# Optimization experiments

Hardware: AMD Instinct MI355X
Metric: run time of the kernel (lower is better)

The kernel has to match this reference:

```python
import jax, jax.numpy as jnp
import numpy as np

B, S, D = 4, 2048, 1024

def setup_inputs() -> dict:
    key = jax.random.key(0)
    ks = jax.random.split(key, 7)
    sc = 1.0 / np.sqrt(D)
    return {
        "x": jax.random.normal(ks[0], (B, S, D), dtype=jnp.float32),
        "Wq": jax.random.normal(ks[1], (D, D), dtype=jnp.float32) * sc,
        "bq": jax.random.normal(ks[2], (D,), dtype=jnp.float32) * 0.01,
        "Wk": jax.random.normal(ks[3], (D, D), dtype=jnp.float32) * sc,
        "bk": jax.random.normal(ks[4], (D,), dtype=jnp.float32) * 0.01,
        "Wv": jax.random.normal(ks[5], (D, D), dtype=jnp.float32) * sc,
        "bv": jax.random.normal(ks[6], (D,), dtype=jnp.float32) * 0.01,
    }

def reference(x, Wq, bq, Wk, bk, Wv, bv):
    # q, k, v: [B, S, D] projections (torch Linear: x @ W^T + b; here W stored as [in, out])
    q = jnp.einsum("bsd,df->bsf", x, Wq) + bq
    k = jnp.einsum("bsd,df->bsf", x, Wk) + bk
    v = jnp.einsum("bsd,df->bsf", x, Wv) + bv
    dim = x.shape[-1]
    # scores: [B, S, S], scaled by sqrt(full d_model) as in the source
    scores = jnp.einsum("bqd,bkd->bqk", q, k) / jnp.sqrt(jnp.float32(dim)).astype(x.dtype)
    attn = jax.nn.softmax(scores, axis=-1)
    return jnp.einsum("bqk,bkd->bqd", attn, v)
```

## Files before the change

kernel.cpp:

```cpp
#include <hip/hip_runtime.h>
#include <hip/hip_bf16.h>

typedef __attribute__((ext_vector_type(8))) short bf16x8;
typedef __attribute__((ext_vector_type(4))) float f32x4;
typedef unsigned short u16;

__device__ __forceinline__ u16 f2bf(float f) {
  unsigned int u = __builtin_bit_cast(unsigned int, f);
  u += 0x7fffu + ((u >> 16) & 1u);
  return (u16)(u >> 16);
}
__device__ __forceinline__ float bf2f(unsigned int h) {
  unsigned int u = h << 16;
  return __builtin_bit_cast(float, u);
}

__device__ __forceinline__ void gload_lds16(const void* g, void* l) {
  __builtin_amdgcn_global_load_lds(
      (const __attribute__((address_space(1))) void*)g,
      (__attribute__((address_space(3))) void*)l, 16, 0, 0);
}

#define BAR() __builtin_amdgcn_s_barrier()
#define VMC(N) asm volatile("s_waitcnt vmcnt(%0)" ::"n"(N) : "memory")

template <int EPI>
__global__ __launch_bounds__(512, 2) void gemm2t(
    const u16* __restrict__ Abase, const u16* __restrict__ Btbase,
    const float* __restrict__ p0, float* __restrict__ p1,
    const float* __restrict__ p2, void* __restrict__ out0,
    void* __restrict__ out1, int Kd, int ldc, long long sAz, long long sBz,
    long long sCz) {
  constexpr int ASZ = 16384;
  constexpr int BSZ = 32768;
  constexpr int BBASE = 2 * ASZ;
  __shared__ char lds[2 * ASZ + 3 * BSZ];

  const int gx = gridDim.x, gy = gridDim.y;
  const int nwg = gx * gy * gridDim.z;
  const int orig = blockIdx.x + gx * (blockIdx.y + gy * blockIdx.z);
  const int q = nwg >> 3, r = nwg & 7;
  const int xcd = orig & 7, loc = orig >> 3;
  const int wgid =
      (xcd < r ? xcd * (q + 1) : r * (q + 1) + (xcd - r) * q) + loc;
  const int bxi = wgid % gx;
  const int byi = (wgid / gx) % gy;
  const int z = wgid / (gx * gy);

  const int tid = threadIdx.x;
  const int w = tid >> 6, l = tid & 63;
  const int wr = w >> 2, wc = w & 3;
  const int lq = l >> 4, lr = l & 15;
  const int bm = byi * 128, bn = bxi * 256;
  const u16* A = Abase + (size_t)z * sAz;
  const u16* Bt = Btbase + (size_t)z * sBz;
  const int NT = Kd >> 6;

  const int kbp = ((tid & 7) ^ ((tid >> 3) & 7)) * 8;
  const int drow = tid >> 3;
  const u16* gA[2];
  const u16* gB[4];
#pragma unroll
  for (int u = 0; u < 2; ++u)
    gA[u] = A + (size_t)(bm + u * 64 + drow) * Kd + kbp;
#pragma unroll
  for (int u = 0; u < 4; ++u)
    gB[u] = Bt + (size_t)(bn + u * 64 + drow) * Kd + kbp;

  auto stageA = [&](int kt) {
    char* d = lds + (kt & 1) * ASZ + tid * 16;
#pragma unroll
    for (int u = 0; u < 2; ++u) gload_lds16(gA[u] + kt * 64, d + u * 8192);
  };
  auto stageB = [&](int kt) {
    char* d = lds + BBASE + (kt % 3) * BSZ + tid * 16;
#pragma unroll
    for (int u = 0; u < 4; ++u) gload_lds16(gB[u] + kt * 64, d + u * 8192);
  };

  const int rA = wr * 64 + lr;
  const int rB0 = wc * 64 + lr;
  int aoff[2];
#pragma unroll
  for (int kh = 0; kh < 2; ++kh)
    aoff[kh] = rA * 128 + (((kh * 4 + lq) ^ (rA & 7)) << 4);

  f32x4 acc[4][2][2] = {};
  bf16x8 a[2][4];
  bf16x8 bb[2][2][2];

  auto rdA = [&](int kt) {
    const char* p = lds + (kt & 1) * ASZ;
#pragma unroll
    for (int kh = 0; kh < 2; ++kh)
#pragma unroll
      for (int mf = 0; mf < 4; ++mf)
        a[kh][mf] = *(const bf16x8*)(p + aoff[kh] + mf * 2048);
  };
  auto rdB = [&](int kt) {
    const char* p = lds + BBASE + (kt % 3) * BSZ;
#pragma unroll
    for (int nh = 0; nh < 2; ++nh) {
      const int rB = rB0 + nh * 32;
#pragma unroll
      for (int kh = 0; kh < 2; ++kh) {
        const int o = rB * 128 + (((kh * 4 + lq) ^ (rB & 7)) << 4);
#pragma unroll
        for (int nf = 0; nf < 2; ++nf)
          bb[nh][kh][nf] = *(const bf16x8*)(p + o + nf * 2048);
      }
    }
  };
  auto mma = [&](int kh) {
    __builtin_amdgcn_s_setprio(1);
#pragma unroll
    for (int nh = 0; nh < 2; ++nh)
#pragma unroll
      for (int mf = 0; mf < 4; ++mf)
#pragma unroll
        for (int nf = 0; nf < 2; ++nf)
          acc[mf][nh][nf] = __builtin_amdgcn_mfma_f32_16x16x32_bf16(
              a[kh][mf], bb[nh][kh][nf], acc[mf][nh][nf], 0, 0, 0);
    __builtin_amdgcn_s_setprio(0);
  };

  stageB(0);
  stageA(0);
  stageB(1);
  stageA(1);
  VMC(6);
  BAR();

  for (int t = 0; t < NT; ++t) {
    rdA(t);
    rdB(t);
    if (t + 2 < NT) stageB(t + 2);
    BAR();
    mma(0);
    if (t + 2 < NT) VMC(4); else VMC(0);
    BAR();
    if (t + 2 < NT) stageA(t + 2);
    mma(1);
  }

  if constexpr (EPI == 4) {
    constexpr float K2 = 0.045084834f;
    u16* C = (u16*)out0 + (size_t)z * sCz;
    const float* cc = p0 + z * 2048;
    float* rs = p1 + z * 2048;
    float psum[4][4] = {};
#pragma unroll
    for (int nh = 0; nh < 2; ++nh)
#pragma unroll
      for (int nf = 0; nf < 2; ++nf) {
        const int col = bn + wc * 64 + nh * 32 + nf * 16 + lr;
        const float cj2 = cc[col];
#pragma unroll
        for (int mf = 0; mf < 4; ++mf) {
          const int row = bm + wr * 64 + mf * 16 + lq * 4;
#pragma unroll
          for (int e = 0; e < 4; ++e) {
            const float pv = exp2f(fmaf(acc[mf][nh][nf][e], K2, cj2));
            C[(size_t)(row + e) * ldc + col] = f2bf(pv);
            psum[mf][e] += pv;
          }
        }
      }
#pragma unroll
    for (int off = 1; off <= 8; off <<= 1)
#pragma unroll
      for (int mf = 0; mf < 4; ++mf)
#pragma unroll
        for (int e = 0; e < 4; ++e)
          psum[mf][e] += __shfl_xor(psum[mf][e], off, 64);
    if (lr == 0) {
#pragma unroll
      for (int mf = 0; mf < 4; ++mf)
#pragma unroll
        for (int e = 0; e < 4; ++e)
          atomicAdd(&rs[bm + wr * 64 + mf * 16 + lq * 4 + e], psum[mf][e]);
    }
  } else if constexpr (EPI == 5) {
    float* C = (float*)out0 + (size_t)z * sCz;
    const float* rs = p1 + z * 2048;
#pragma unroll
    for (int nh = 0; nh < 2; ++nh)
#pragma unroll
      for (int nf = 0; nf < 2; ++nf) {
        const int col = bn + wc * 64 + nh * 32 + nf * 16 + lr;
#pragma unroll
        for (int mf = 0; mf < 4; ++mf) {
          const int row = bm + wr * 64 + mf * 16 + lq * 4;
#pragma unroll
          for (int e = 0; e < 4; ++e)
            C[(size_t)(row + e) * ldc + col] =
                acc[mf][nh][nf][e] / rs[row + e];
        }
      }
  } else {
    const int mat = bn >> 10;
    u16* T = (u16*)out0;
    u16* V = (u16*)out1;
#pragma unroll
    for (int nh = 0; nh < 2; ++nh)
#pragma unroll
      for (int nf = 0; nf < 2; ++nf) {
        const int oc = (bn + wc * 64 + nh * 32 + nf * 16 + lr) & 1023;
        if (mat == 0) {
#pragma unroll
          for (int mf = 0; mf < 4; ++mf) {
            const int row = bm + wr * 64 + mf * 16 + lq * 4;
#pragma unroll
            for (int e = 0; e < 4; ++e)
              T[(size_t)(row + e) * 1024 + oc] = f2bf(acc[mf][nh][nf][e]);
          }
        } else {
          const float bb2 = p2[oc];
#pragma unroll
          for (int mf = 0; mf < 4; ++mf) {
            const int row = bm + wr * 64 + mf * 16 + lq * 4;
            const int bz = row >> 11, sdx = row & 2047;
            ushort4 pk;
            pk.x = f2bf(acc[mf][nh][nf][0] + bb2);
            pk.y = f2bf(acc[mf][nh][nf][1] + bb2);
            pk.z = f2bf(acc[mf][nh][nf][2] + bb2);
            pk.w = f2bf(acc[mf][nh][nf][3] + bb2);
            *(ushort4*)&V[((size_t)bz * 1024 + oc) * 2048 + sdx] = pk;
          }
        }
      }
  }
}

__global__ __launch_bounds__(256) void gemmM(
    const u16* __restrict__ Abase, const u16* __restrict__ Btbase,
    float* __restrict__ out0, int Kd, int Kext, int ldc, long long sAz,
    long long sBz, long long sCz) {
  constexpr int ASZ = 16384;
  constexpr int BSZ = 16384;
  constexpr int BBASE = 2 * ASZ;
  __shared__ char lds[2 * ASZ + 3 * BSZ];

  const int tid = threadIdx.x;
  const int w = tid >> 6, l = tid & 63;
  const int wr = w >> 1, wc = w & 1;
  const int lq = l >> 4, lr = l & 15;
  const int bm = blockIdx.y * 128, bn = blockIdx.x * 128;
  const int z = blockIdx.z;
  const u16* A = Abase + (size_t)z * sAz;
  const u16* Bt = Btbase + (size_t)z * sBz;
  const int NT = Kext >> 6;

  const int kbp = ((tid & 7) ^ ((tid >> 3) & 7)) * 8;
  const int drow = tid >> 3;
  const u16* gA[4];
  const u16* gB[4];
#pragma unroll
  for (int u = 0; u < 4; ++u) {
    gA[u] = A + (size_t)(bm + u * 32 + drow) * Kd + kbp;
    gB[u] = Bt + (size_t)(bn + u * 32 + drow) * Kd + kbp;
  }

  auto stageA = [&](int kt) {
    char* d = lds + (kt & 1) * ASZ + tid * 16;
#pragma unroll
    for (int u = 0; u < 4; ++u) gload_lds16(gA[u] + kt * 64, d + u * 4096);
  };
  auto stageB = [&](int kt) {
    char* d = lds + BBASE + (kt % 3) * BSZ + tid * 16;
#pragma unroll
    for (int u = 0; u < 4; ++u) gload_lds16(gB[u] + kt * 64, d + u * 4096);
  };

  const int rA = wr * 64 + lr;
  const int rB0 = wc * 64 + lr;
  int aoff[2];
#pragma unroll
  for (int kh = 0; kh < 2; ++kh)
    aoff[kh] = rA * 128 + (((kh * 4 + lq) ^ (rA & 7)) << 4);

  f32x4 acc[4][2][2] = {};
  bf16x8 a[2][4];
  bf16x8 bb[2][2][2];

  auto rdA = [&](int kt) {
    const char* p = lds + (kt & 1) * ASZ;
#pragma unroll
    for (int kh = 0; kh < 2; ++kh)
#pragma unroll
      for (int mf = 0; mf < 4; ++mf)
        a[kh][mf] = *(const bf16x8*)(p + aoff[kh] + mf * 2048);
  };
  auto rdB = [&](int kt) {
    const char* p = lds + BBASE + (kt % 3) * BSZ;
#pragma unroll
    for (int nh = 0; nh < 2; ++nh) {
      const int rB = rB0 + nh * 32;
#pragma unroll
      for (int kh = 0; kh < 2; ++kh) {
        const int o = rB * 128 + (((kh * 4 + lq) ^ (rB & 7)) << 4);
#pragma unroll
        for (int nf = 0; nf < 2; ++nf)
          bb[nh][kh][nf] = *(const bf16x8*)(p + o + nf * 2048);
      }
    }
  };
  auto mma = [&](int kh) {
#pragma unroll
    for (int nh = 0; nh < 2; ++nh)
#pragma unroll
      for (int mf = 0; mf < 4; ++mf)
#pragma unroll
        for (int nf = 0; nf < 2; ++nf)
          acc[mf][nh][nf] = __builtin_amdgcn_mfma_f32_16x16x32_bf16(
              a[kh][mf], bb[nh][kh][nf], acc[mf][nh][nf], 0, 0, 0);
  };

  stageB(0);
  stageA(0);
  stageB(1);
  stageA(1);
  VMC(8);
  BAR();

  for (int t = 0; t < NT; ++t) {
    rdA(t);
    rdB(t);
    if (t + 2 < NT) stageB(t + 2);
    BAR();
    mma(0);
    if (t + 2 < NT) VMC(4); else VMC(0);
    BAR();
    if (t + 2 < NT) stageA(t + 2);
    mma(1);
  }

  float* C = out0 + (size_t)z * sCz;
#pragma unroll
  for (int nh = 0; nh < 2; ++nh)
#pragma unroll
    for (int nf = 0; nf < 2; ++nf) {
      const int col = bn + wc * 64 + nh * 32 + nf * 16 + lr;
#pragma unroll
      for (int mf = 0; mf < 4; ++mf) {
        const int row = bm + wr * 64 + mf * 16 + lq * 4;
#pragma unroll
        for (int e = 0; e < 4; ++e)
          C[(size_t)(row + e) * ldc + col] = acc[mf][nh][nf][e];
      }
    }
}

__global__ __launch_bounds__(256) void prep(
    const float* __restrict__ x, const float* __restrict__ Wq,
    const float* __restrict__ Wk, const float* __restrict__ Wv,
    const float* __restrict__ bq, u16* __restrict__ xb,
    u16* __restrict__ Wqb, u16* __restrict__ Wkb, u16* __restrict__ WtTV,
    float* __restrict__ vvec) {
  const int bid = blockIdx.x;
  const int tid = threadIdx.x;
  if (bid < 8192) {
    const int i = bid * 256 + tid;
    const float4 v = ((const float4*)x)[i];
    ushort4 o;
    o.x = f2bf(v.x);
    o.y = f2bf(v.y);
    o.z = f2bf(v.z);
    o.w = f2bf(v.w);
    ((ushort4*)xb)[i] = o;
  } else if (bid < 11264) {
    const int b = bid - 8192;
    const int zz = b >> 10, t2 = b & 1023;
    const int k0 = (t2 >> 5) * 32, n0 = (t2 & 31) * 32;
    const int tx = tid & 31, ty0 = tid >> 5;
    if (zz == 2) {
      __shared__ float s[32][33];
#pragma unroll
      for (int r = 0; r < 4; ++r) {
        const int row = ty0 + 8 * r;
        s[row][tx] = Wv[(size_t)(k0 + row) * 1024 + n0 + tx];
      }
      __syncthreads();
#pragma unroll
      for (int r = 0; r < 4; ++r) {
        const int row = ty0 + 8 * r;
        WtTV[1048576 + (size_t)(n0 + row) * 1024 + k0 + tx] =
            f2bf(s[tx][row]);
      }
    } else {
      const float* W = zz ? Wk : Wq;
      u16* O = zz ? Wkb : Wqb;
#pragma unroll
      for (int r = 0; r < 4; ++r) {
        const size_t i = (size_t)(k0 + ty0 + 8 * r) * 1024 + n0 + tx;
        O[i] = f2bf(W[i]);
      }
    }
  } else {
    const int d = bid - 11264;
    const float4 wv = ((const float4*)(Wk + (size_t)d * 1024))[tid];
    const float4 bv = ((const float4*)bq)[tid];
    float p = wv.x * bv.x + wv.y * bv.y + wv.z * bv.z + wv.w * bv.w;
#pragma unroll
    for (int o = 32; o; o >>= 1) p += __shfl_xor(p, o, 64);
    __shared__ float red[4];
    if ((tid & 63) == 0) red[tid >> 6] = p;
    __syncthreads();
    if (tid == 0) vvec[d] = red[0] + red[1] + red[2] + red[3];
  }
}

__global__ __launch_bounds__(256) void mck(const float* __restrict__ Mf,
                                           u16* __restrict__ Mt,
                                           const u16* __restrict__ xb,
                                           const float* __restrict__ v,
                                           float* __restrict__ c,
                                           float* __restrict__ rowsum) {
  const int bid = blockIdx.x;
  const int tid = threadIdx.x;
  if (bid < 1024) {
    const int i = bid * 256 + tid;
    const float4 a = ((const float4*)Mf)[i];
    const float4 b = ((const float4*)(Mf + 1048576))[i];
    const float4 cc = ((const float4*)(Mf + 2097152))[i];
    const float4 d = ((const float4*)(Mf + 3145728))[i];
    ushort4 o;
    o.x = f2bf(a.x + b.x + cc.x + d.x);
    o.y = f2bf(a.y + b.y + cc.y + d.y);
    o.z = f2bf(a.z + b.z + cc.z + d.z);
    o.w = f2bf(a.w + b.w + cc.w + d.w);
    ((ushort4*)Mt)[i] = o;
  } else {
    const int b2 = bid - 1024;
    if (b2 < 32) rowsum[b2 * 256 + tid] = 0.f;
    const int j = b2 * 8 + (tid >> 5);
    const int lane = tid & 31;
    const u16* xr = xb + (size_t)j * 1024;
    float p = 0.f;
#pragma unroll
    for (int k = 0; k < 4; ++k) {
      const int g = k * 32 + lane;
      const uint4 u = ((const uint4*)xr)[g];
      const float4 v0 = ((const float4*)v)[g * 2];
      const float4 v1 = ((const float4*)v)[g * 2 + 1];
      p += bf2f(u.x & 0xffffu) * v0.x + bf2f(u.x >> 16) * v0.y +
           bf2f(u.y & 0xffffu) * v0.z + bf2f(u.y >> 16) * v0.w +
           bf2f(u.z & 0xffffu) * v1.x + bf2f(u.z >> 16) * v1.y +
           bf2f(u.w & 0xffffu) * v1.z + bf2f(u.w >> 16) * v1.w;
    }
#pragma unroll
    for (int o = 16; o; o >>= 1) p += __shfl_xor(p, o, 64);
    if (lane == 0) c[j] = p * 0.045084834f;
  }
}

extern "C" void kernel_launch(void* const* d_in, const int* in_sizes, int n_in,
                              void* d_out, int out_size, void* d_ws,
                              size_t ws_size, hipStream_t stream) {
  const float* x = (const float*)d_in[0];
  const float* Wq = (const float*)d_in[1];
  const float* bq = (const float*)d_in[2];
  const float* Wk = (const float*)d_in[3];
  const float* Wv = (const float*)d_in[5];
  const float* bv = (const float*)d_in[6];
  float* out = (float*)d_out;
  char* ws = (char*)d_ws;

  u16* xb = (u16*)ws;
  u16* WtTV = (u16*)(ws + 16777216);
  u16* Wqb = (u16*)(ws + 20971520);
  u16* Wkb = (u16*)(ws + 23068672);
  float* vvec = (float*)(ws + 25165824);
  float* cvec = (float*)(ws + 25169920);
  float* rowsum = (float*)(ws + 25202688);
  float* Mf32 = (float*)(ws + 25235456);
  u16* T = (u16*)(ws + 25235456);
  u16* Vt = (u16*)(ws + 42012672);
  u16* SP = (u16*)(ws + 58789888);

  prep<<<12288, 256, 0, stream>>>(x, Wq, Wk, Wv, bq, xb, Wqb, Wkb, WtTV,
                                  vvec);

  gemmM<<<dim3(8, 8, 4), 256, 0, stream>>>(Wkb, Wqb, Mf32, 1024, 256, 1024,
                                           256LL, 256LL, 1048576LL);

  mck<<<2048, 256, 0, stream>>>(Mf32, WtTV, xb, vvec, cvec, rowsum);

  gemm2t<7><<<dim3(8, 64, 1), 512, 0, stream>>>(
      xb, WtTV, nullptr, nullptr, bv, T, Vt, 1024, 0, 0, 0, 0);

  gemm2t<4><<<dim3(8, 16, 4), 512, 0, stream>>>(
      T, xb, cvec, rowsum, nullptr, SP, nullptr, 1024, 2048, 2097152LL,
      2097152LL, 4194304LL);

  gemm2t<5><<<dim3(4, 16, 4), 512, 0, stream>>>(
      SP, Vt, nullptr, rowsum, nullptr, out, nullptr, 2048, 1024, 4194304LL,
      2097152LL, 2097152LL);
}
```

Measured before the change: 164.7 us.

## Replace score GEMM with 256x256-tile kernel using quarter-phased double-buffered LDS

The score GEMM (T times x transposed, followed by the exp and row-sum epilogue) moves from the generic gemm2t<4> kernel to a dedicated gemm8q kernel. gemm8q uses 256x256 output tiles, double-buffered LDS for the A and B halves, and loads staged across four sub-phases per k-tile, interleaved with MFMA groups at raised priority. This is meant to raise arithmetic intensity and overlap global-to-LDS copies with compute, cutting global traffic per FLOP. The cost is more accumulator registers per thread (32 f32x4) and half as many workgroups (256), which may hurt occupancy or load balance.

```diff
diff --git a/kernel.cpp b/kernel.cpp
--- a/kernel.cpp
+++ b/kernel.cpp
@@ -23,6 +23,156 @@
 
 #define BAR() __builtin_amdgcn_s_barrier()
 #define VMC(N) asm volatile("s_waitcnt vmcnt(%0)" ::"n"(N) : "memory")
+
+__global__ __launch_bounds__(512, 2) void gemm8q(
+    const u16* __restrict__ Abase, const u16* __restrict__ Btbase,
+    const float* __restrict__ cc_all, float* __restrict__ rs_all,
+    u16* __restrict__ outp, int Kd, int ldc, long long sAz, long long sBz,
+    long long sCz) {
+  constexpr int HSZ = 16384;
+  constexpr int BUFSZ = 4 * HSZ;
+  __shared__ char lds[2 * BUFSZ];
+
+  const int gx = gridDim.x, gy = gridDim.y;
+  const int nwg = gx * gy * gridDim.z;
+  const int orig = blockIdx.x + gx * (blockIdx.y + gy * blockIdx.z);
+  const int q = nwg >> 3, r = nwg & 7;
+  const int xcd = orig & 7, loc = orig >> 3;
+  const int wgid =
+      (xcd < r ? xcd * (q + 1) : r * (q + 1) + (xcd - r) * q) + loc;
+  const int bxi = wgid % gx;
+  const int byi = (wgid / gx) % gy;
+  const int z = wgid / (gx * gy);
+
+  const int tid = threadIdx.x;
+  const int w = tid >> 6, l = tid & 63;
+  const int wr = w >> 2, wc = w & 3;
+  const int lq = l >> 4, lr = l & 15;
+  const int bm = byi * 256, bn = bxi * 256;
+  const u16* A = Abase + (size_t)z * sAz;
+  const u16* Bt = Btbase + (size_t)z * sBz;
+  const int NT = Kd >> 6;
+
+  const int kbp = ((tid & 7) ^ ((tid >> 3) & 7)) * 8;
+  const int drow = tid >> 3;
+  const u16* gA[2][2];
+  const u16* gB[2][2];
+#pragma unroll
+  for (int h = 0; h < 2; ++h)
+#pragma unroll
+    for (int u = 0; u < 2; ++u) {
+      gA[h][u] = A + (size_t)(bm + h * 128 + u * 64 + drow) * Kd + kbp;
+      gB[h][u] = Bt + (size_t)(bn + h * 128 + u * 64 + drow) * Kd + kbp;
+    }
+  auto stageA = [&](int buf, int h, int kt) {
+    char* d = lds + buf * BUFSZ + h * HSZ + tid * 16;
+    gload_lds16(gA[h][0] + kt * 64, d);
+    gload_lds16(gA[h][1] + kt * 64, d + 8192);
+  };
+  auto stageB = [&](int buf, int h, int kt) {
+    char* d = lds + buf * BUFSZ + (2 + h) * HSZ + tid * 16;
+    gload_lds16(gB[h][0] + kt * 64, d);
+    gload_lds16(gB[h][1] + kt * 64, d + 8192);
+  };
+
+  const int ah = wr;
+  const int bh = wc >> 1;
+  const int bc0 = (wc & 1) * 64;
+  const int sel = lr & 7;
+  int koff[2];
+#pragma unroll
+  for (int kh = 0; kh < 2; ++kh) koff[kh] = (((kh * 4 + lq) ^ sel) << 4);
+
+  f32x4 acc[8][4] = {};
+  bf16x8 bb[4][2];
+  bf16x8 a[2][2];
+
+  stageA(0, 0, 0);
+  stageA(0, 1, 0);
+  stageB(0, 0, 0);
+  stageB(0, 1, 0);
+  stageA(1, 0, 1);
+  stageA(1, 1, 1);
+  stageB(1, 0, 1);
+  stageB(1, 1, 1);
+  VMC(8);
+  BAR();
+
+  for (int u = 0; u < NT; ++u) {
+    const int buf = u & 1, obuf = buf ^ 1;
+#pragma unroll
+    for (int qp = 0; qp < 4; ++qp) {
+      const char* pA = lds + buf * BUFSZ + ah * HSZ;
+#pragma unroll
+      for (int mf2 = 0; mf2 < 2; ++mf2)
+#pragma unroll
+        for (int kh = 0; kh < 2; ++kh)
+          a[mf2][kh] = *(const bf16x8*)(pA + (qp * 32 + mf2 * 16 + lr) * 128 +
+                                        koff[kh]);
+      if (qp == 0) {
+        const char* pB = lds + buf * BUFSZ + (2 + bh) * HSZ;
+#pragma unroll
+        for (int nf = 0; nf < 4; ++nf)
+#pragma unroll
+          for (int kh = 0; kh < 2; ++kh)
+            bb[nf][kh] = *(const bf16x8*)(pB + (bc0 + nf * 16 + lr) * 128 +
+                                          koff[kh]);
+      }
+      if (qp == 0 && u >= 1 && u + 1 < NT) stageA(obuf, 0, u + 1);
+      if (qp == 1 && u >= 1 && u + 1 < NT) stageA(obuf, 1, u + 1);
+      if (qp == 2 && u + 2 < NT) stageB(buf, 0, u + 2);
+      if (qp == 3 && u + 2 < NT) stageB(buf, 1, u + 2);
+      BAR();
+      __builtin_amdgcn_s_setprio(1);
+#pragma unroll
+      for (int kh = 0; kh < 2; ++kh)
+#pragma unroll
+        for (int mf2 = 0; mf2 < 2; ++mf2)
+#pragma unroll
+          for (int nf = 0; nf < 4; ++nf)
+            acc[qp * 2 + mf2][nf] = __builtin_amdgcn_mfma_f32_16x16x32_bf16(
+                a[mf2][kh], bb[nf][kh], acc[qp * 2 + mf2][nf], 0, 0, 0);
+      __builtin_amdgcn_s_setprio(0);
+      if (qp == 3) {
+        if (u + 2 < NT) {
+          VMC(4);
+        } else if (u + 1 < NT) {
+          VMC(0);
+        }
+      }
+      BAR();
+    }
+  }
+
+  constexpr float K2 = 0.045084834f;
+  u16* C = outp + (size_t)z * sCz;
+  const float* cc = cc_all + z * 2048;
+  float* rs = rs_all + z * 2048;
+#pragma unroll
+  for (int mf = 0; mf < 8; ++mf) {
+    const int row = bm + wr * 128 + mf * 16 + lq * 4;
+    float ps[4] = {0.f, 0.f, 0.f, 0.f};
+#pragma unroll
+    for (int nf = 0; nf < 4; ++nf) {
+      const int col = bn + wc * 64 + nf * 16 + lr;
+      const float cj2 = cc[col];
+#pragma unroll
+      for (int e = 0; e < 4; ++e) {
+        const float pv = exp2f(fmaf(acc[mf][nf][e], K2, cj2));
+        C[(size_t)(row + e) * ldc + col] = f2bf(pv);
+        ps[e] += pv;
+      }
+    }
+#pragma unroll
+    for (int off = 1; off <= 8; off <<= 1)
+#pragma unroll
+      for (int e = 0; e < 4; ++e) ps[e] += __shfl_xor(ps[e], off, 64);
+    if (lr == 0) {
+#pragma unroll
+      for (int e = 0; e < 4; ++e) atomicAdd(&rs[row + e], ps[e]);
+    }
+  }
+}
 
 template <int EPI>
 __global__ __launch_bounds__(512, 2) void gemm2t(
@@ -143,44 +293,7 @@
     mma(1);
   }
 
-  if constexpr (EPI == 4) {
-    constexpr float K2 = 0.045084834f;
-    u16* C = (u16*)out0 + (size_t)z * sCz;
-    const float* cc = p0 + z * 2048;
-    float* rs = p1 + z * 2048;
-    float psum[4][4] = {};
-#pragma unroll
-    for (int nh = 0; nh < 2; ++nh)
-#pragma unroll
-      for (int nf = 0; nf < 2; ++nf) {
-        const int col = bn + wc * 64 + nh * 32 + nf * 16 + lr;
-        const float cj2 = cc[col];
-#pragma unroll
-        for (int mf = 0; mf < 4; ++mf) {
-          const int row = bm + wr * 64 + mf * 16 + lq * 4;
-#pragma unroll
-          for (int e = 0; e < 4; ++e) {
-            const float pv = exp2f(fmaf(acc[mf][nh][nf][e], K2, cj2));
-            C[(size_t)(row + e) * ldc + col] = f2bf(pv);
-            psum[mf][e] += pv;
-          }
-        }
-      }
-#pragma unroll
-    for (int off = 1; off <= 8; off <<= 1)
-#pragma unroll
-      for (int mf = 0; mf < 4; ++mf)
-#pragma unroll
-        for (int e = 0; e < 4; ++e)
-          psum[mf][e] += __shfl_xor(psum[mf][e], off, 64);
-    if (lr == 0) {
-#pragma unroll
-      for (int mf = 0; mf < 4; ++mf)
-#pragma unroll
-        for (int e = 0; e < 4; ++e)
-          atomicAdd(&rs[bm + wr * 64 + mf * 16 + lq * 4 + e], psum[mf][e]);
-    }
-  } else if constexpr (EPI == 5) {
+  if constexpr (EPI == 5) {
     float* C = (float*)out0 + (size_t)z * sCz;
     const float* rs = p1 + z * 2048;
 #pragma unroll
@@ -489,9 +602,9 @@
   gemm2t<7><<<dim3(8, 64, 1), 512, 0, stream>>>(
       xb, WtTV, nullptr, nullptr, bv, T, Vt, 1024, 0, 0, 0, 0);
 
-  gemm2t<4><<<dim3(8, 16, 4), 512, 0, stream>>>(
-      T, xb, cvec, rowsum, nullptr, SP, nullptr, 1024, 2048, 2097152LL,
-      2097152LL, 4194304LL);
+  gemm8q<<<dim3(8, 8, 4), 512, 0, stream>>>(T, xb, cvec, rowsum, SP, 1024,
+                                            2048, 2097152LL, 2097152LL,
+                                            4194304LL);
 
   gemm2t<5><<<dim3(4, 16, 4), 512, 0, stream>>>(
       SP, Vt, nullptr, rowsum, nullptr, out, nullptr, 2048, 1024, 4194304LL,
```

New measurement: 157.0 us. 1.05x faster.
